# Performance work log

Hardware: AMD Instinct MI355X
Metric: run time of the kernel (lower is better)

The kernel has to match this reference:

```python
import jax, jax.numpy as jnp
import numpy as np


def _conv(x, w, padding):
    # x: NCHW, w: OIHW
    return jax.lax.conv_general_dilated(
        x, w, window_strides=(1, 1), padding=padding,
        dimension_numbers=('NCHW', 'OIHW', 'NCHW'))


def setup_inputs() -> dict:
    key = jax.random.key(0)
    ks = jax.random.split(key, 4)
    B, Cin, H, W = 128, 1024, 14, 14
    planes, expansion = 256, 4
    x = jax.random.normal(ks[0], (B, Cin, H, W), dtype=jnp.float32)
    # conv weights (layouts are fully dense since rho=0.0)
    w1 = jax.random.normal(ks[1], (planes, Cin, 1, 1), dtype=jnp.float32) * 0.02
    w2 = jax.random.normal(ks[2], (planes, planes, 3, 3), dtype=jnp.float32) * 0.02
    w3 = jax.random.normal(ks[3], (planes * expansion, planes, 1, 1), dtype=jnp.float32) * 0.02
    # Fixup scalar biases / scale
    z = jnp.zeros((1,), dtype=jnp.float32)
    return {
        'x': x, 'w1': w1, 'w2': w2, 'w3': w3,
        'bias1b': z, 'bias2a': z, 'bias2b': z, 'bias3a': z, 'bias3b': z,
        'rscale': jnp.ones((1,), dtype=jnp.float32), 'rbias': z,
    }


def reference(x, w1, w2, w3, bias1b, bias2a, bias2b, bias3a, bias3b, rscale, rbias):
    # conv1(x) + bias1b  (1x1, fused output bias)
    out = _conv(x, w1, 'VALID') + bias1b[0]
    # conv2(out + bias2a) + bias2b  (3x3, pad 1, fused input+output bias)
    out = _conv(out + bias2a[0], w2, 'SAME') + bias2b[0]
    # conv3(out + bias3a) + bias3b  (1x1)
    out = _conv(out + bias3a[0], w3, 'VALID') + bias3b[0]
    # fused scale + bias + residual ReLU: relu(out*rscale + rbias + identity)
    return jax.nn.relu(out * rscale[0] + rbias[0] + x)
```

## Files before the change

### kernel.cpp

```cpp
#include <hip/hip_runtime.h>
#include <stdint.h>

typedef __bf16 bf16x8 __attribute__((ext_vector_type(8)));
typedef float f32x4 __attribute__((ext_vector_type(4)));
typedef unsigned short u16;

__device__ __forceinline__ u16 f2bf(float f){
  uint32_t u = __float_as_uint(f);
  u = (u + 0x7fffu + ((u >> 16) & 1u)) >> 16;
  return (u16)u;
}

__device__ __forceinline__ void gl_lds16(const void* g, void* l){
  __builtin_amdgcn_global_load_lds((const __attribute__((address_space(1))) void*)g,
                                   (__attribute__((address_space(3))) void*)l, 16, 0, 0);
}

__global__ void cvt_f32_bf16(const float* __restrict__ in, u16* __restrict__ out, int n){
  int i = blockIdx.x*256 + threadIdx.x;
  if (i < n) out[i] = f2bf(in[i]);
}

__global__ void prep_w2k(const float* __restrict__ in, u16* __restrict__ out){
  int i = blockIdx.x*256 + threadIdx.x;
  if (i < 589824){
    int o = i / 2304, r = i - o*2304, kq = r >> 8, c = r & 255;
    out[i] = f2bf(in[((size_t)o*256 + c)*9 + kq]);
  }
}

__global__ __launch_bounds__(256) void transform_x(const float* __restrict__ x,
                                                   u16* __restrict__ xp0){
  __shared__ float lds[64*201];
  const int b = blockIdx.y, c0 = blockIdx.x*64, t = threadIdx.x;
  const float4* src = (const float4*)x + (size_t)b*50176 + (size_t)c0*49;
  #pragma unroll
  for (int r = 0; r < 13; ++r){
    int q = r*256 + t;
    if (q < 3136){
      unsigned c = (unsigned)q / 49u, f = (unsigned)q - c*49u;
      float4 v = src[q];
      float* d = &lds[c*201 + f*4];
      d[0]=v.x; d[1]=v.y; d[2]=v.z; d[3]=v.w;
    }
  }
  __syncthreads();
  const int c4 = (t & 15)*4, pg = t >> 4;
  #pragma unroll
  for (int r = 0; r < 13; ++r){
    int p = r*16 + pg;
    if (p < 196){
      ushort4 pk;
      ((u16*)&pk)[0] = f2bf(lds[(c4+0)*201 + p]);
      ((u16*)&pk)[1] = f2bf(lds[(c4+1)*201 + p]);
      ((u16*)&pk)[2] = f2bf(lds[(c4+2)*201 + p]);
      ((u16*)&pk)[3] = f2bf(lds[(c4+3)*201 + p]);
      *(ushort4*)&xp0[((size_t)b*196 + p)*1024 + c0 + c4] = pk;
    }
  }
}

__global__ void zfill_borders(u16* __restrict__ xp1){
  int tid = blockIdx.x*256 + threadIdx.x;
  int row_i = tid >> 5, w = tid & 31;
  unsigned b = (unsigned)row_i / 60u, k = (unsigned)row_i - b*60u;
  int y, xx;
  if (k < 32){ y = (k>>4)*15; xx = k & 15; }
  else if (k < 46){ y = k - 31; xx = 0; }
  else { y = k - 45; xx = 15; }
  size_t row = (size_t)b*256 + y*16 + xx;
  ((ulonglong2*)(xp1 + row*256))[w] = (ulonglong2){0,0};
}

template<int CID>
__global__ __launch_bounds__(256, (CID==3) ? 4 : 3) void gemm_k(
    const u16* __restrict__ A, const u16* __restrict__ B,
    u16* __restrict__ Obf, float* __restrict__ Of32, const float* __restrict__ xres,
    const float* __restrict__ s0, const float* __restrict__ s1, const float* __restrict__ s2)
{
  constexpr int KTOT  = (CID==1) ? 1024 : (CID==2) ? 2304 : 256;
  constexpr int NSTEP = KTOT / 64;
  constexpr int BN    = (CID==3) ? 128 : 64;
  constexpr int WN    = (CID==3) ? 64 : 32;
  constexpr int NJ    = WN / 16;
  constexpr int NBG   = BN*8/256;
  constexpr int BUFB  = 16384 + BN*128;
  constexpr size_t LDSZ = (CID==3) ? 33792 : 2*(size_t)BUFB;

  __shared__ char lds[LDSZ];
  const int t    = threadIdx.x;
  const int lane = t & 63;
  const int w    = t >> 6;
  const int wm   = (w >> 1) * 64, wn = (w & 1) * WN;
  const int m0   = blockIdx.y * 128, n0 = blockIdx.x * BN;

  f32x4 acc[4][NJ] = {};

  uint32_t aoff[4], boff[NBG];
  #pragma unroll
  for (int i = 0; i < 4; ++i){
    int gl = i*256 + t, row = gl >> 3, ss = gl & 7;
    int xo = (ss ^ (row & 7)) << 4;
    aoff[i] = (uint32_t)(m0 + row) * (KTOT*2) + xo;
  }
  #pragma unroll
  for (int i = 0; i < NBG; ++i){
    int gl = i*256 + t, row = gl >> 3, ss = gl & 7;
    int xo = (ss ^ (row & 7)) << 4;
    uint32_t n = n0 + row;
    if constexpr (CID==1)      boff[i] = n * 2048u + xo;
    else if constexpr (CID==3) boff[i] = n * 512u + xo;
    else {
      uint32_t b = n / 196u, p = n - b*196u;
      uint32_t py = p / 14u,  px = p - py*14u;
      uint32_t prow = b*256u + (py+1)*16u + (px+1);
      boff[i] = prow * 512u + xo;
    }
  }

  auto stage = [&](int buf, int s){
    char* Ab = lds + buf*BUFB;
    char* Bb = Ab + 16384;
    const int ka = s*128;
    int kb;
    if constexpr (CID==2){
      int kq = s >> 2;
      kb = ((kq/3 - 1)*16 + (kq%3) - 1)*512 + (s & 3)*128;
    } else kb = ka;
    #pragma unroll
    for (int i = 0; i < 4; ++i)
      gl_lds16((const char*)A + aoff[i] + ka, Ab + (i*256 + t)*16);
    #pragma unroll
    for (int i = 0; i < NBG; ++i)
      gl_lds16((const char*)B + (int64_t)boff[i] + kb, Bb + (i*256 + t)*16);
  };

  auto compute = [&](int buf){
    char* Ab = lds + buf*BUFB;
    char* Bb = Ab + 16384;
    #pragma unroll
    for (int h = 0; h < 2; ++h){
      bf16x8 af[4], bfr[NJ];
      #pragma unroll
      for (int i = 0; i < 4; ++i){
        int row = wm + i*16 + (lane & 15);
        af[i] = *(const bf16x8*)(Ab + row*128 + (((h*4 + (lane>>4)) ^ (row & 7)) << 4));
      }
      #pragma unroll
      for (int j = 0; j < NJ; ++j){
        int row = wn + j*16 + (lane & 15);
        bfr[j] = *(const bf16x8*)(Bb + row*128 + (((h*4 + (lane>>4)) ^ (row & 7)) << 4));
      }
      #pragma unroll
      for (int i = 0; i < 4; ++i)
        #pragma unroll
        for (int j = 0; j < NJ; ++j)
          acc[i][j] = __builtin_amdgcn_mfma_f32_16x16x32_bf16(af[i], bfr[j], acc[i][j], 0, 0, 0);
    }
  };

  if constexpr (CID==3){
    #pragma unroll
    for (int s = 0; s < NSTEP; ++s){
      if (s) __syncthreads();
      stage(0, s);
      __syncthreads();
      compute(0);
    }
  } else {
    stage(0, 0);
    __syncthreads();
    for (int s = 0; s < NSTEP; ++s){
      if (s + 1 < NSTEP) stage((s+1) & 1, s+1);
      compute(s & 1);
      __syncthreads();
    }
  }

  if constexpr (CID==1 || CID==2){
    float badd = s0[0] + s1[0];
    #pragma unroll
    for (int i = 0; i < 4; ++i){
      int o = m0 + wm + i*16 + ((lane >> 4) << 2);
      #pragma unroll
      for (int j = 0; j < NJ; ++j){
        uint32_t n = n0 + wn + j*16 + (lane & 15);
        size_t rn;
        if constexpr (CID==1){
          uint32_t b = n / 196u, p = n - b*196u;
          uint32_t py = p / 14u, px = p - py*14u;
          rn = (size_t)b*256 + (py+1)*16 + (px+1);
        } else rn = n;
        ushort4 pk;
        #pragma unroll
        for (int q = 0; q < 4; ++q) ((u16*)&pk)[q] = f2bf(acc[i][j][q] + badd);
        *(ushort4*)(Obf + rn*256 + o) = pk;
      }
    }
  } else {
    float b3 = s0[0], rs = s1[0], rbv = s2[0];
    float* ldsF = (float*)lds;
    #pragma unroll
    for (int pass = 0; pass < 2; ++pass){
      __syncthreads();
      if ((wm >> 6) == pass){
        #pragma unroll
        for (int i = 0; i < 4; ++i){
          int rb = i*16 + ((lane >> 4) << 2);
          #pragma unroll
          for (int j = 0; j < 4; ++j){
            int col = wn + j*16 + (lane & 15);
            #pragma unroll
            for (int q = 0; q < 4; ++q) ldsF[(rb + q)*132 + col] = acc[i][j][q];
          }
        }
      }
      __syncthreads();
      #pragma unroll
      for (int r = 0; r < 8; ++r){
        int row = (w << 4) + ((lane >> 5) << 3) + r;
        int n4  = (lane & 31) << 2;
        float4 v = *(float4*)&ldsF[row*132 + n4];
        uint32_t n = n0 + n4;
        uint32_t b = n / 196u, p = n - b*196u;
        int o = m0 + pass*64 + row;
        size_t base = ((size_t)b*1024 + o)*196 + p;
        float4 xr = *(const float4*)&xres[base];
        float4 ov;
        ov.x = fmaxf((v.x + b3)*rs + rbv + xr.x, 0.f);
        ov.y = fmaxf((v.y + b3)*rs + rbv + xr.y, 0.f);
        ov.z = fmaxf((v.z + b3)*rs + rbv + xr.z, 0.f);
        ov.w = fmaxf((v.w + b3)*rs + rbv + xr.w, 0.f);
        *(float4*)&Of32[base] = ov;
      }
    }
  }
}

extern "C" void kernel_launch(void* const* d_in, const int* in_sizes, int n_in,
                              void* d_out, int out_size, void* d_ws, size_t ws_size,
                              hipStream_t stream){
  (void)in_sizes; (void)n_in; (void)out_size; (void)ws_size;
  const float* x   = (const float*)d_in[0];
  const float* w1  = (const float*)d_in[1];
  const float* w2  = (const float*)d_in[2];
  const float* w3  = (const float*)d_in[3];
  const float* b1b = (const float*)d_in[4];
  const float* b2a = (const float*)d_in[5];
  const float* b2b = (const float*)d_in[6];
  const float* b3a = (const float*)d_in[7];
  const float* b3b = (const float*)d_in[8];
  const float* rsc = (const float*)d_in[9];
  const float* rbi = (const float*)d_in[10];

  char* ws  = (char*)d_ws;
  u16*  xp1 = (u16*)ws;
  u16*  xp2 = (u16*)(ws + 16777216);
  u16*  wb1 = (u16*)(ws + 29622272);
  u16*  wb2 = (u16*)(ws + 30146560);
  u16*  wb3 = (u16*)(ws + 31326208);
  u16*  xp0 = (u16*)d_out;

  cvt_f32_bf16<<<dim3(1024), 256, 0, stream>>>(w1, wb1, 262144);
  prep_w2k    <<<dim3(2304), 256, 0, stream>>>(w2, wb2);
  cvt_f32_bf16<<<dim3(1024), 256, 0, stream>>>(w3, wb3, 262144);
  transform_x <<<dim3(16,128), 256, 0, stream>>>(x, xp0);
  zfill_borders<<<dim3(960), 256, 0, stream>>>(xp1);

  gemm_k<1><<<dim3(392, 2), 256, 0, stream>>>(wb1, xp0, xp1, nullptr, nullptr, b1b, b2a, nullptr);
  gemm_k<2><<<dim3(392, 2), 256, 0, stream>>>(wb2, xp1, xp2, nullptr, nullptr, b2b, b3a, nullptr);
  gemm_k<3><<<dim3(196, 8), 256, 0, stream>>>(wb3, xp2, nullptr, (float*)d_out, x, b3b, rsc, rbi);
}
```

Before: 341.3 us.

## Remap GEMM blocks per XCD, fuse prep kernels, read residual from bf16

Result: faster. 331.9 us (-2.7%).

```diff
diff --git a/kernel.cpp b/kernel.cpp
--- a/kernel.cpp
+++ b/kernel.cpp
@@ -10,22 +10,37 @@
   u = (u + 0x7fffu + ((u >> 16) & 1u)) >> 16;
   return (u16)u;
 }
-
+__device__ __forceinline__ float bf2f(u16 v){
+  return __uint_as_float(((uint32_t)v) << 16);
+}
 __device__ __forceinline__ void gl_lds16(const void* g, void* l){
   __builtin_amdgcn_global_load_lds((const __attribute__((address_space(1))) void*)g,
                                    (__attribute__((address_space(3))) void*)l, 16, 0, 0);
 }
 
-__global__ void cvt_f32_bf16(const float* __restrict__ in, u16* __restrict__ out, int n){
-  int i = blockIdx.x*256 + threadIdx.x;
-  if (i < n) out[i] = f2bf(in[i]);
-}
-
-__global__ void prep_w2k(const float* __restrict__ in, u16* __restrict__ out){
-  int i = blockIdx.x*256 + threadIdx.x;
-  if (i < 589824){
+__global__ __launch_bounds__(256) void prep_all(
+    const float* __restrict__ w1, const float* __restrict__ w2,
+    const float* __restrict__ w3, u16* __restrict__ wb1, u16* __restrict__ wb2,
+    u16* __restrict__ wb3, u16* __restrict__ xp1){
+  int bid = blockIdx.x, t = threadIdx.x;
+  if (bid < 1024){
+    int i = bid*256 + t; wb1[i] = f2bf(w1[i]);
+  } else if (bid < 3328){
+    int i = (bid-1024)*256 + t;
     int o = i / 2304, r = i - o*2304, kq = r >> 8, c = r & 255;
-    out[i] = f2bf(in[((size_t)o*256 + c)*9 + kq]);
+    wb2[i] = f2bf(w2[((size_t)o*256 + c)*9 + kq]);
+  } else if (bid < 4352){
+    int i = (bid-3328)*256 + t; wb3[i] = f2bf(w3[i]);
+  } else {
+    int tid = (bid-4352)*256 + t;
+    int row_i = tid >> 5, w = tid & 31;
+    unsigned b = (unsigned)row_i / 60u, k = (unsigned)row_i - b*60u;
+    int y, xx;
+    if (k < 32){ y = (k>>4)*15; xx = k & 15; }
+    else if (k < 46){ y = k - 31; xx = 0; }
+    else { y = k - 45; xx = 15; }
+    size_t row = (size_t)b*256 + y*16 + xx;
+    ((ulonglong2*)(xp1 + row*256))[w] = (ulonglong2){0,0};
   }
 }
 
@@ -60,22 +75,10 @@
   }
 }
 
-__global__ void zfill_borders(u16* __restrict__ xp1){
-  int tid = blockIdx.x*256 + threadIdx.x;
-  int row_i = tid >> 5, w = tid & 31;
-  unsigned b = (unsigned)row_i / 60u, k = (unsigned)row_i - b*60u;
-  int y, xx;
-  if (k < 32){ y = (k>>4)*15; xx = k & 15; }
-  else if (k < 46){ y = k - 31; xx = 0; }
-  else { y = k - 45; xx = 15; }
-  size_t row = (size_t)b*256 + y*16 + xx;
-  ((ulonglong2*)(xp1 + row*256))[w] = (ulonglong2){0,0};
-}
-
 template<int CID>
-__global__ __launch_bounds__(256, (CID==3) ? 4 : 3) void gemm_k(
+__device__ __forceinline__ void gemm_body(
     const u16* __restrict__ A, const u16* __restrict__ B,
-    u16* __restrict__ Obf, float* __restrict__ Of32, const float* __restrict__ xres,
+    u16* __restrict__ Obf, float* __restrict__ Of32, const u16* __restrict__ xresb,
     const float* __restrict__ s0, const float* __restrict__ s1, const float* __restrict__ s2)
 {
   constexpr int KTOT  = (CID==1) ? 1024 : (CID==2) ? 2304 : 256;
@@ -85,14 +88,19 @@
   constexpr int NJ    = WN / 16;
   constexpr int NBG   = BN*8/256;
   constexpr int BUFB  = 16384 + BN*128;
-  constexpr size_t LDSZ = (CID==3) ? 33792 : 2*(size_t)BUFB;
+  constexpr int LDSZ  = (CID==3) ? 33792 : 2*BUFB;
 
   __shared__ char lds[LDSZ];
   const int t    = threadIdx.x;
   const int lane = t & 63;
   const int w    = t >> 6;
   const int wm   = (w >> 1) * 64, wn = (w & 1) * WN;
-  const int m0   = blockIdx.y * 128, n0 = blockIdx.x * BN;
+
+  const int orig = blockIdx.x;
+  const int bid  = (orig & 7) * ((int)gridDim.x >> 3) + (orig >> 3);
+  int n0, m0;
+  if constexpr (CID==3){ n0 = (bid >> 3) * 128; m0 = (bid & 7) * 128; }
+  else                 { n0 = (bid >> 1) * 64;  m0 = (bid & 1) * 128; }
 
   f32x4 acc[4][NJ] = {};
 
@@ -225,16 +233,33 @@
         uint32_t b = n / 196u, p = n - b*196u;
         int o = m0 + pass*64 + row;
         size_t base = ((size_t)b*1024 + o)*196 + p;
-        float4 xr = *(const float4*)&xres[base];
+        const u16* xr = xresb + (size_t)n*1024 + o;
         float4 ov;
-        ov.x = fmaxf((v.x + b3)*rs + rbv + xr.x, 0.f);
-        ov.y = fmaxf((v.y + b3)*rs + rbv + xr.y, 0.f);
-        ov.z = fmaxf((v.z + b3)*rs + rbv + xr.z, 0.f);
-        ov.w = fmaxf((v.w + b3)*rs + rbv + xr.w, 0.f);
+        ov.x = fmaxf((v.x + b3)*rs + rbv + bf2f(xr[0]),    0.f);
+        ov.y = fmaxf((v.y + b3)*rs + rbv + bf2f(xr[1024]), 0.f);
+        ov.z = fmaxf((v.z + b3)*rs + rbv + bf2f(xr[2048]), 0.f);
+        ov.w = fmaxf((v.w + b3)*rs + rbv + bf2f(xr[3072]), 0.f);
         *(float4*)&Of32[base] = ov;
       }
     }
   }
+}
+
+__global__ __launch_bounds__(256, 3) void gemm1_conv(
+    const u16* __restrict__ A, const u16* __restrict__ B, u16* __restrict__ O,
+    const float* __restrict__ s0, const float* __restrict__ s1){
+  gemm_body<1>(A, B, O, nullptr, nullptr, s0, s1, nullptr);
+}
+__global__ __launch_bounds__(256, 3) void gemm2_conv(
+    const u16* __restrict__ A, const u16* __restrict__ B, u16* __restrict__ O,
+    const float* __restrict__ s0, const float* __restrict__ s1){
+  gemm_body<2>(A, B, O, nullptr, nullptr, s0, s1, nullptr);
+}
+__global__ __launch_bounds__(256, 4) void gemm3_conv(
+    const u16* __restrict__ A, const u16* __restrict__ B, const u16* __restrict__ xresb,
+    float* __restrict__ O, const float* __restrict__ s0, const float* __restrict__ s1,
+    const float* __restrict__ s2){
+  gemm_body<3>(A, B, nullptr, O, xresb, s0, s1, s2);
 }
 
 extern "C" void kernel_launch(void* const* d_in, const int* in_sizes, int n_in,
@@ -256,18 +281,15 @@
   char* ws  = (char*)d_ws;
   u16*  xp1 = (u16*)ws;
   u16*  xp2 = (u16*)(ws + 16777216);
-  u16*  wb1 = (u16*)(ws + 29622272);
-  u16*  wb2 = (u16*)(ws + 30146560);
-  u16*  wb3 = (u16*)(ws + 31326208);
-  u16*  xp0 = (u16*)d_out;
-
-  cvt_f32_bf16<<<dim3(1024), 256, 0, stream>>>(w1, wb1, 262144);
-  prep_w2k    <<<dim3(2304), 256, 0, stream>>>(w2, wb2);
-  cvt_f32_bf16<<<dim3(1024), 256, 0, stream>>>(w3, wb3, 262144);
-  transform_x <<<dim3(16,128), 256, 0, stream>>>(x, xp0);
-  zfill_borders<<<dim3(960), 256, 0, stream>>>(xp1);
-
-  gemm_k<1><<<dim3(392, 2), 256, 0, stream>>>(wb1, xp0, xp1, nullptr, nullptr, b1b, b2a, nullptr);
-  gemm_k<2><<<dim3(392, 2), 256, 0, stream>>>(wb2, xp1, xp2, nullptr, nullptr, b2b, b3a, nullptr);
-  gemm_k<3><<<dim3(196, 8), 256, 0, stream>>>(wb3, xp2, nullptr, (float*)d_out, x, b3b, rsc, rbi);
-}
+  u16*  xp0 = (u16*)(ws + 29622272);
+  u16*  wb1 = (u16*)(ws + 81002496);
+  u16*  wb2 = (u16*)(ws + 81526784);
+  u16*  wb3 = (u16*)(ws + 82706432);
+
+  prep_all   <<<dim3(5312),   256, 0, stream>>>(w1, w2, w3, wb1, wb2, wb3, xp1);
+  transform_x<<<dim3(16,128), 256, 0, stream>>>(x, xp0);
+
+  gemm1_conv<<<dim3(784),  256, 0, stream>>>(wb1, xp0, xp1, b1b, b2a);
+  gemm2_conv<<<dim3(784),  256, 0, stream>>>(wb2, xp1, xp2, b2b, b3a);
+  gemm3_conv<<<dim3(1568), 256, 0, stream>>>(wb3, xp2, xp0, (float*)d_out, b3b, rsc, rbi);
+}
```
